# Optimization experiments

Measured on AMD Instinct MI355X. Metric: run time of the kernel, lower is better.

Reference implementation:

```python
import jax, jax.numpy as jnp
import numpy as np

NUM_CLASSES = 2047
TIME_WEIGHT = 2.0
EOS_COEF = 0.1
B, Q, N = 64, 100, 16


def _lsa(cost):
    """Jonker-Volgenant min-cost assignment for rectangular cost [R, C], R <= C.
    Returns (row_ind, col_ind) with row_ind = arange(R). Equivalent to
    scipy.optimize.linear_sum_assignment."""
    R, Cn = cost.shape
    u = np.zeros(R + 1)
    v = np.zeros(Cn + 1)
    p = np.zeros(Cn + 1, dtype=np.int64)  # p[j] = 1-based row matched to col j (0 = free)
    for i in range(1, R + 1):
        p[0] = i
        j0 = 0
        minv = np.full(Cn + 1, np.inf)
        used = np.zeros(Cn + 1, dtype=bool)
        way = np.zeros(Cn + 1, dtype=np.int64)
        while True:
            used[j0] = True
            i0 = p[j0]
            cur = cost[i0 - 1] - u[i0] - v[1:]
            free = ~used[1:]
            upd = free & (cur < minv[1:])
            minv[1:] = np.where(upd, cur, minv[1:])
            way[1:] = np.where(upd, j0, way[1:])
            j1 = int(np.argmin(np.where(free, minv[1:], np.inf))) + 1
            delta = minv[j1]
            u[p[used]] += delta
            v[used] -= delta
            minv[1:] = np.where(free, minv[1:] - delta, minv[1:])
            j0 = j1
            if p[j0] == 0:
                break
        while j0 != 0:  # augment along the alternating path
            j1 = way[j0]
            p[j0] = p[j1]
            j0 = j1
    col4row = np.zeros(R, dtype=np.int64)
    for j in range(1, Cn + 1):
        if p[j] > 0:
            col4row[p[j] - 1] = j - 1
    return np.arange(R), col4row


def _match(C):
    """C: np.ndarray [B, Q, N]. Returns (query_idx [B,N], target_idx [B,N])."""
    b, q, n = C.shape
    qs = np.zeros((b, n), np.int64)
    ts = np.zeros((b, n), np.int64)
    for i in range(b):
        r, c = _lsa(C[i].T)  # rows = targets (N), cols = queries (Q); N <= Q
        ts[i] = r
        qs[i] = c
    return qs, ts


def setup_inputs() -> dict:
    key = jax.random.key(0)
    k1, k2, k3, k4 = jax.random.split(key, 4)
    pred_logits = jax.random.normal(k1, (B, Q, NUM_CLASSES + 1), dtype=jnp.float32)
    pred_time = jax.random.uniform(k2, (B, Q, 1), dtype=jnp.float32)
    labels = jax.random.randint(k3, (B, N), 1, NUM_CLASSES + 1)  # class 0 = no-object
    timestamps = jax.random.uniform(k4, (B, N, 1), dtype=jnp.float32)
    return {"pred_logits": pred_logits, "pred_time": pred_time,
            "labels": labels, "timestamps": timestamps}


def reference(pred_logits, pred_time, labels, timestamps):
    b, q = pred_logits.shape[:2]
    n = labels.shape[1]
    # --- Hungarian matching cost (detached, host-side assignment as in the original) ---
    probs = jax.nn.softmax(pred_logits, axis=-1)                              # [B,Q,C+1]
    cost_class = -jnp.take_along_axis(probs, labels[:, None, :], axis=2)      # [B,Q,N]
    cost_time = jnp.abs(pred_time[..., 0][:, :, None] -
                        timestamps[..., 0][:, None, :])                       # [B,Q,N] (cdist p=1)
    C = cost_class + TIME_WEIGHT * cost_time
    Cnp = np.nan_to_num(np.asarray(jax.device_get(C)),
                        nan=100.0, posinf=100.0, neginf=-100.0)
    qs, ts = _match(Cnp)
    qs_j = jnp.asarray(qs)  # matched query indices  [B,N]
    ts_j = jnp.asarray(ts)  # matched target indices [B,N]
    # --- weighted cross entropy over all queries ---
    class_ids = jnp.take_along_axis(labels, ts_j, axis=1)                     # [B,N]
    batch_ar = jnp.arange(b)[:, None]
    target_classes = jnp.zeros((b, q), dtype=jnp.int64).at[batch_ar, qs_j].set(class_ids)
    logZ = jax.nn.logsumexp(pred_logits, axis=-1)                             # [B,Q]
    tgt_logit = jnp.take_along_axis(pred_logits, target_classes[..., None], axis=2)[..., 0]
    nll = logZ - tgt_logit                                                    # [B,Q]
    ce_w = jnp.ones(NUM_CLASSES + 1, jnp.float32).at[0].set(EOS_COEF)
    w = ce_w[target_classes]
    loss_ce = jnp.sum(w * nll) / jnp.sum(w)
    # --- L1 loss on matched timestamps ---
    matched_pred = pred_time[batch_ar, qs_j, 0]                               # [B,N]
    matched_tgt = jnp.take_along_axis(timestamps[..., 0], ts_j, axis=1)       # [B,N]
    loss_time = jnp.mean(jnp.abs(matched_pred - matched_tgt))
    return loss_ce + TIME_WEIGHT * loss_time
```

## Files before the change

### kernel.cpp

```cpp
#include <hip/hip_runtime.h>
#include <hip/hip_bf16.h>
#include <math.h>

#define BB 64
#define QQ 100
#define NN 16
#define CC 2048
#define TIME_WEIGHT 2.0f
#define EOS_COEF 0.1f

__device__ __forceinline__ double readlane_d(double x, int lane) {
    int lo = __builtin_amdgcn_readlane(__double2loint(x), lane);
    int hi = __builtin_amdgcn_readlane(__double2hiint(x), lane);
    return __hiloint2double(hi, lo);
}

template <int CTRL>
__device__ __forceinline__ double dpp_fmin_f64(double x) {
    int lo_s = __double2loint(x), hi_s = __double2hiint(x);
    int lo = __builtin_amdgcn_update_dpp(lo_s, lo_s, CTRL, 0xF, 0xF, false);
    int hi = __builtin_amdgcn_update_dpp(hi_s, hi_s, CTRL, 0xF, 0xF, false);
    return fmin(x, __hiloint2double(hi, lo));
}

__global__ __launch_bounds__(256) void lse_cost_kernel(
    const float* __restrict__ logits, const float* __restrict__ ptime,
    const int* __restrict__ labels, const float* __restrict__ tstamp,
    float* __restrict__ logZ, float* __restrict__ Cg,
    float* __restrict__ lsepart, float* __restrict__ sums, int* __restrict__ counter)
{
    if (blockIdx.x == 0 && threadIdx.x == 0) {
        sums[0] = 0.f; sums[1] = 0.f; *counter = 0;
    }
    const int wave = threadIdx.x >> 6;
    const int lane = threadIdx.x & 63;
    const int bq = blockIdx.x * 4 + wave;
    const int b = bq / QQ, q = bq % QQ;
    const float4* row4 = (const float4*)(logits + (size_t)bq * CC);

    float4 v[8];
    #pragma unroll
    for (int c = 0; c < 8; ++c) v[c] = row4[c * 64 + lane];

    float m = -INFINITY;
    #pragma unroll
    for (int c = 0; c < 8; ++c)
        m = fmaxf(m, fmaxf(fmaxf(v[c].x, v[c].y), fmaxf(v[c].z, v[c].w)));
    #pragma unroll
    for (int s = 1; s < 64; s <<= 1) m = fmaxf(m, __shfl_xor(m, s, 64));

    float sum = 0.f;
    #pragma unroll
    for (int c = 0; c < 8; ++c)
        sum += expf(v[c].x - m) + expf(v[c].y - m) +
               expf(v[c].z - m) + expf(v[c].w - m);
    #pragma unroll
    for (int s = 1; s < 64; s <<= 1) sum += __shfl_xor(sum, s, 64);

    const float lz = m + logf(sum);
    if (lane == 0) logZ[bq] = lz;

    const float pt = ptime[bq];
    if (lane < NN) {
        int lab = labels[b * NN + lane];
        float lg = logits[(size_t)bq * CC + lab];
        float cc = -expf(lg - lz);
        float ct = fabsf(pt - tstamp[b * NN + lane]);
        float val = cc + TIME_WEIGHT * ct;
        if (isnan(val)) val = 100.0f;
        else if (isinf(val)) val = (val > 0.f) ? 100.0f : -100.0f;
        Cg[((size_t)b * NN + lane) * QQ + q] = val;
    }

    __shared__ float red[4];
    if (lane == 0) red[wave] = lz - logits[(size_t)bq * CC];
    __syncthreads();
    if (threadIdx.x == 0)
        lsepart[blockIdx.x] = red[0] + red[1] + red[2] + red[3];
}

__global__ __launch_bounds__(64) void hungarian_kernel(
    const float* __restrict__ Cg, const float* __restrict__ logits,
    const float* __restrict__ ptime, const int* __restrict__ labels,
    const float* __restrict__ tstamp, const float* __restrict__ logZ,
    const float* __restrict__ lsepart, float* __restrict__ sums,
    int* __restrict__ counter, float* __restrict__ out)
{
    const int b = blockIdx.x;
    const int t = threadIdx.x;

    __shared__ float costS[NN * QQ];
    __shared__ int qsl[NN];

    const float* cgb = Cg + (size_t)b * NN * QQ;
    #pragma unroll
    for (int k = 0; k < 25; ++k) costS[k * 64 + t] = cgb[k * 64 + t];
    __syncthreads();

    const int jc0 = t + 1;
    const int jc1 = t + 65;
    const bool has2 = (jc1 <= QQ);
    const int t2 = has2 ? (t + 64) : t;

    double v0 = 0.0, v1 = 0.0;
    double ureg = 0.0;
    int preg0 = 0, preg1 = 0;
    const double INF = __builtin_inf();

    for (int i = 1; i <= NN; ++i) {
        double minv0 = INF, minv1 = INF;
        bool used0 = false, used1 = false;
        int way0 = 0, way1 = 0;
        bool inTree = (t == i - 1);
        int j0 = 0;
        int i0 = i;

        while (true) {
            used0 |= (j0 == jc0);
            used1 |= (j0 == jc1);
            inTree = inTree || (t == i0 - 1);
            const double u_i0 = readlane_d(ureg, i0 - 1);

            const int rowbase = (i0 - 1) * QQ;
            const double ca = (double)costS[rowbase + t];
            const double cb = (double)costS[rowbase + t2];

            if (!used0) {
                double cur = ca - u_i0 - v0;
                if (cur < minv0) { minv0 = cur; way0 = j0; }
            }
            if (has2 && !used1) {
                double cur = cb - u_i0 - v1;
                if (cur < minv1) { minv1 = cur; way1 = j0; }
            }

            double m0 = used0 ? INF : minv0;
            double m1 = (has2 && !used1) ? minv1 : INF;
            double gmin = fmin(m0, m1);
            gmin = dpp_fmin_f64<0xB1>(gmin);
            gmin = dpp_fmin_f64<0x4E>(gmin);
            gmin = dpp_fmin_f64<0x124>(gmin);
            gmin = dpp_fmin_f64<0x128>(gmin);
            {
                double h0 = readlane_d(gmin, 0);
                double h1 = readlane_d(gmin, 16);
                double h2 = readlane_d(gmin, 32);
                double h3 = readlane_d(gmin, 48);
                gmin = fmin(fmin(h0, h1), fmin(h2, h3));
            }
            unsigned long long A  = __ballot(!used0 && (minv0 == gmin));
            unsigned long long Bm = __ballot(has2 && !used1 && (minv1 == gmin));
            int j1 = (A != 0ull) ? ((int)__builtin_ctzll(A) + 1)
                                 : ((int)__builtin_ctzll(Bm) + 65);
            const double delta = gmin;

            if (inTree) ureg += delta;
            if (used0) v0 -= delta; else minv0 -= delta;
            if (has2) { if (used1) v1 -= delta; else minv1 -= delta; }

            j0 = j1;
            int pj = (j0 <= 64) ? __builtin_amdgcn_readlane(preg0, j0 - 1)
                                : __builtin_amdgcn_readlane(preg1, j0 - 65);
            if (pj == 0) break;
            i0 = pj;
        }

        while (j0 != 0) {
            int jn = (j0 <= 64) ? __builtin_amdgcn_readlane(way0, j0 - 1)
                                : __builtin_amdgcn_readlane(way1, j0 - 65);
            int pv;
            if (jn == 0) pv = i;
            else pv = (jn <= 64) ? __builtin_amdgcn_readlane(preg0, jn - 1)
                                 : __builtin_amdgcn_readlane(preg1, jn - 65);
            if (j0 == jc0) preg0 = pv;
            if (has2 && j0 == jc1) preg1 = pv;
            j0 = jn;
        }
    }

    if (preg0 > 0) qsl[preg0 - 1] = jc0 - 1;
    if (has2 && preg1 > 0) qsl[preg1 - 1] = jc1 - 1;
    __syncthreads();

    float corr = 0.f, tl = 0.f;
    if (t < NN) {
        int qcol = qsl[t];
        int lab = labels[b * NN + t];
        int bq = b * QQ + qcol;
        float lz = logZ[bq];
        float lgm = logits[(size_t)bq * CC + lab];
        float lg0 = logits[(size_t)bq * CC];
        corr = (lz - lgm) - EOS_COEF * (lz - lg0);
        tl = fabsf(ptime[bq] - tstamp[b * NN + t]);
    }
    #pragma unroll
    for (int s = 1; s < 64; s <<= 1) {
        corr += __shfl_xor(corr, s, 64);
        tl   += __shfl_xor(tl, s, 64);
    }

    int old = 0;
    if (t == 0) {
        atomicAdd(&sums[0], corr);
        atomicAdd(&sums[1], tl);
        __threadfence();
        old = atomicAdd(counter, 1);
    }
    old = __shfl(old, 0, 64);
    if (old == BB - 1) {
        __threadfence();
        float r0 = 0.f;
        #pragma unroll
        for (int k = 0; k < 25; ++k) r0 += lsepart[t + 64 * k];
        #pragma unroll
        for (int s = 1; s < 64; s <<= 1) r0 += __shfl_xor(r0, s, 64);
        if (t == 0) {
            float s0 = atomicAdd(&sums[0], 0.0f);
            float s1 = atomicAdd(&sums[1], 0.0f);
            const float sum_w = (float)(BB * NN) * 1.0f
                              + (float)(BB * (QQ - NN)) * EOS_COEF;
            float loss_ce = (EOS_COEF * r0 + s0) / sum_w;
            float loss_t  = s1 / (float)(BB * NN);
            out[0] = loss_ce + TIME_WEIGHT * loss_t;
        }
    }
}

extern "C" void kernel_launch(void* const* d_in, const int* in_sizes, int n_in,
                              void* d_out, int out_size, void* d_ws, size_t ws_size,
                              hipStream_t stream) {
    const float* logits = (const float*)d_in[0];
    const float* ptime  = (const float*)d_in[1];
    const int*   labels = (const int*)d_in[2];
    const float* tstamp = (const float*)d_in[3];
    float* out = (float*)d_out;

    char* ws = (char*)d_ws;
    float* logZ    = (float*)ws;
    float* Cg      = (float*)(ws + 25600);
    float* lsepart = (float*)(ws + 435200);
    float* sums    = (float*)(ws + 441600);
    int*   counter = (int*)(ws + 441608);

    lse_cost_kernel<<<1600, 256, 0, stream>>>(logits, ptime, labels, tstamp,
                                              logZ, Cg, lsepart, sums, counter);
    hungarian_kernel<<<BB, 64, 0, stream>>>(Cg, logits, ptime, labels, tstamp,
                                            logZ, lsepart, sums, counter, out);
}
```

Baseline: 105.4 us.

## Fuse LSE/cost and Hungarian kernels via per-batch last-block election

Merges the two kernels into one launch. The last of the 25 blocks that finish a batch's cost rows, detected with a per-batch atomic counter, runs the Hungarian assignment for that batch. The cost tile is staged as a float2 layout so each lane gets both of its columns in one LDS read. Global atomic sums are replaced by per-batch slots plus a final reduction, and counters are cleared with a memset. This removes a kernel launch and the tail serialization between stages, and lets the assignment of early batches overlap with LSE work on later ones, at the cost of an extra memset node and fence-based cross-block synchronization.

```diff
diff --git a/kernel.cpp b/kernel.cpp
--- a/kernel.cpp
+++ b/kernel.cpp
@@ -23,21 +23,24 @@
     return fmin(x, __hiloint2double(hi, lo));
 }
 
-__global__ __launch_bounds__(256) void lse_cost_kernel(
+__device__ __forceinline__ float load_agent(const float* p) {
+    return __hip_atomic_load((float*)p, __ATOMIC_RELAXED, __HIP_MEMORY_SCOPE_AGENT);
+}
+
+__global__ __launch_bounds__(256) void fused_kernel(
     const float* __restrict__ logits, const float* __restrict__ ptime,
     const int* __restrict__ labels, const float* __restrict__ tstamp,
     float* __restrict__ logZ, float* __restrict__ Cg,
-    float* __restrict__ lsepart, float* __restrict__ sums, int* __restrict__ counter)
+    float* __restrict__ lsepart, float* __restrict__ corrB,
+    float* __restrict__ tlB, int* __restrict__ bcnt,
+    int* __restrict__ counter, float* __restrict__ out)
 {
-    if (blockIdx.x == 0 && threadIdx.x == 0) {
-        sums[0] = 0.f; sums[1] = 0.f; *counter = 0;
-    }
     const int wave = threadIdx.x >> 6;
     const int lane = threadIdx.x & 63;
     const int bq = blockIdx.x * 4 + wave;
     const int b = bq / QQ, q = bq % QQ;
+
     const float4* row4 = (const float4*)(logits + (size_t)bq * CC);
-
     float4 v[8];
     #pragma unroll
     for (int c = 0; c < 8; ++c) v[c] = row4[c * 64 + lane];
@@ -73,34 +76,37 @@
     }
 
     __shared__ float red[4];
+    __shared__ int lastFlag;
     if (lane == 0) red[wave] = lz - logits[(size_t)bq * CC];
+
+    __threadfence();
     __syncthreads();
-    if (threadIdx.x == 0)
+    if (threadIdx.x == 0) {
         lsepart[blockIdx.x] = red[0] + red[1] + red[2] + red[3];
-}
-
-__global__ __launch_bounds__(64) void hungarian_kernel(
-    const float* __restrict__ Cg, const float* __restrict__ logits,
-    const float* __restrict__ ptime, const int* __restrict__ labels,
-    const float* __restrict__ tstamp, const float* __restrict__ logZ,
-    const float* __restrict__ lsepart, float* __restrict__ sums,
-    int* __restrict__ counter, float* __restrict__ out)
-{
-    const int b = blockIdx.x;
+        __threadfence();
+        lastFlag = (atomicAdd(&bcnt[b], 1) == 24);
+    }
+    __syncthreads();
+    if (!lastFlag) return;
+    if (threadIdx.x >= 64) return;
+
     const int t = threadIdx.x;
-
-    __shared__ float costS[NN * QQ];
-    __shared__ int qsl[NN];
-
-    const float* cgb = Cg + (size_t)b * NN * QQ;
-    #pragma unroll
-    for (int k = 0; k < 25; ++k) costS[k * 64 + t] = cgb[k * 64 + t];
-    __syncthreads();
+    __threadfence();
 
     const int jc0 = t + 1;
     const int jc1 = t + 65;
     const bool has2 = (jc1 <= QQ);
     const int t2 = has2 ? (t + 64) : t;
+
+    __shared__ float2 costS2[NN][64];
+    const float* cgb = Cg + (size_t)b * NN * QQ;
+    #pragma unroll
+    for (int r = 0; r < NN; ++r) {
+        float a = load_agent(&cgb[r * QQ + t]);
+        float c = load_agent(&cgb[r * QQ + t2]);
+        costS2[r][t] = make_float2(a, c);
+    }
+    asm volatile("s_waitcnt lgkmcnt(0)" ::: "memory");
 
     double v0 = 0.0, v1 = 0.0;
     double ureg = 0.0;
@@ -121,9 +127,9 @@
             inTree = inTree || (t == i0 - 1);
             const double u_i0 = readlane_d(ureg, i0 - 1);
 
-            const int rowbase = (i0 - 1) * QQ;
-            const double ca = (double)costS[rowbase + t];
-            const double cb = (double)costS[rowbase + t2];
+            const float2 cab = costS2[i0 - 1][t];
+            const double ca = (double)cab.x;
+            const double cb = (double)cab.y;
 
             if (!used0) {
                 double cur = ca - u_i0 - v0;
@@ -178,20 +184,21 @@
         }
     }
 
+    __shared__ int qsl[NN];
     if (preg0 > 0) qsl[preg0 - 1] = jc0 - 1;
     if (has2 && preg1 > 0) qsl[preg1 - 1] = jc1 - 1;
-    __syncthreads();
+    asm volatile("s_waitcnt lgkmcnt(0)" ::: "memory");
 
     float corr = 0.f, tl = 0.f;
     if (t < NN) {
         int qcol = qsl[t];
         int lab = labels[b * NN + t];
-        int bq = b * QQ + qcol;
-        float lz = logZ[bq];
-        float lgm = logits[(size_t)bq * CC + lab];
-        float lg0 = logits[(size_t)bq * CC];
-        corr = (lz - lgm) - EOS_COEF * (lz - lg0);
-        tl = fabsf(ptime[bq] - tstamp[b * NN + t]);
+        int bq2 = b * QQ + qcol;
+        float lz2 = load_agent(&logZ[bq2]);
+        float lgm = logits[(size_t)bq2 * CC + lab];
+        float lg0 = logits[(size_t)bq2 * CC];
+        corr = (lz2 - lgm) - EOS_COEF * (lz2 - lg0);
+        tl = fabsf(ptime[bq2] - tstamp[b * NN + t]);
     }
     #pragma unroll
     for (int s = 1; s < 64; s <<= 1) {
@@ -201,8 +208,8 @@
 
     int old = 0;
     if (t == 0) {
-        atomicAdd(&sums[0], corr);
-        atomicAdd(&sums[1], tl);
+        corrB[b] = corr;
+        tlB[b] = tl;
         __threadfence();
         old = atomicAdd(counter, 1);
     }
@@ -211,12 +218,16 @@
         __threadfence();
         float r0 = 0.f;
         #pragma unroll
-        for (int k = 0; k < 25; ++k) r0 += lsepart[t + 64 * k];
+        for (int k = 0; k < 25; ++k)
+            r0 += load_agent(&lsepart[t + 64 * k]);
         #pragma unroll
         for (int s = 1; s < 64; s <<= 1) r0 += __shfl_xor(r0, s, 64);
         if (t == 0) {
-            float s0 = atomicAdd(&sums[0], 0.0f);
-            float s1 = atomicAdd(&sums[1], 0.0f);
+            float s0 = 0.f, s1 = 0.f;
+            for (int i2 = 0; i2 < BB; ++i2) {
+                s0 += load_agent(&corrB[i2]);
+                s1 += load_agent(&tlB[i2]);
+            }
             const float sum_w = (float)(BB * NN) * 1.0f
                               + (float)(BB * (QQ - NN)) * EOS_COEF;
             float loss_ce = (EOS_COEF * r0 + s0) / sum_w;
@@ -239,11 +250,14 @@
     float* logZ    = (float*)ws;
     float* Cg      = (float*)(ws + 25600);
     float* lsepart = (float*)(ws + 435200);
-    float* sums    = (float*)(ws + 441600);
-    int*   counter = (int*)(ws + 441608);
-
-    lse_cost_kernel<<<1600, 256, 0, stream>>>(logits, ptime, labels, tstamp,
-                                              logZ, Cg, lsepart, sums, counter);
-    hungarian_kernel<<<BB, 64, 0, stream>>>(Cg, logits, ptime, labels, tstamp,
-                                            logZ, lsepart, sums, counter, out);
-}
+    float* corrB   = (float*)(ws + 441600);
+    float* tlB     = (float*)(ws + 441856);
+    int*   bcnt    = (int*)(ws + 442112);
+    int*   counter = (int*)(ws + 442368);
+
+    hipMemsetAsync(ws + 442112, 0, 260, stream);
+
+    fused_kernel<<<1600, 256, 0, stream>>>(logits, ptime, labels, tstamp,
+                                           logZ, Cg, lsepart, corrB, tlB,
+                                           bcnt, counter, out);
+}
```

Result: slower. 271.5 us (+157.6%).

## Pack cost rows as per-lane float2 in LDS, drop barriers, pin logits registers

Applied to the files above, without the earlier changes.

The Hungarian kernel now stores each cost row as a per-lane float2 holding both of that lane's columns, so each augmenting step does one 64-bit LDS read instead of two scalar reads. The __syncthreads barriers are replaced with s_waitcnt lgkmcnt(0). That is enough only because the block is a single wave and each lane reads its own LDS slot. In the LSE kernel, empty asm statements pin the loaded logits in VGPRs so the compiler cannot rematerialize or reorder the loads. The asm and barrier removal depend on wave64 single-wave blocks and rely on compiler and hardware behaviour.

```diff
diff --git a/kernel.cpp b/kernel.cpp
--- a/kernel.cpp
+++ b/kernel.cpp
@@ -1,5 +1,4 @@
 #include <hip/hip_runtime.h>
-#include <hip/hip_bf16.h>
 #include <math.h>
 
 #define BB 64
@@ -22,6 +21,16 @@
     int hi = __builtin_amdgcn_update_dpp(hi_s, hi_s, CTRL, 0xF, 0xF, false);
     return fmin(x, __hiloint2double(hi, lo));
 }
+
+#define KEEP_ALIVE_V8(v)                                                     \
+    asm volatile("" : "+v"(v[0].x), "+v"(v[0].y), "+v"(v[0].z), "+v"(v[0].w),\
+                     "+v"(v[1].x), "+v"(v[1].y), "+v"(v[1].z), "+v"(v[1].w),\
+                     "+v"(v[2].x), "+v"(v[2].y), "+v"(v[2].z), "+v"(v[2].w),\
+                     "+v"(v[3].x), "+v"(v[3].y), "+v"(v[3].z), "+v"(v[3].w));\
+    asm volatile("" : "+v"(v[4].x), "+v"(v[4].y), "+v"(v[4].z), "+v"(v[4].w),\
+                     "+v"(v[5].x), "+v"(v[5].y), "+v"(v[5].z), "+v"(v[5].w),\
+                     "+v"(v[6].x), "+v"(v[6].y), "+v"(v[6].z), "+v"(v[6].w),\
+                     "+v"(v[7].x), "+v"(v[7].y), "+v"(v[7].z), "+v"(v[7].w))
 
 __global__ __launch_bounds__(256) void lse_cost_kernel(
     const float* __restrict__ logits, const float* __restrict__ ptime,
@@ -41,6 +50,7 @@
     float4 v[8];
     #pragma unroll
     for (int c = 0; c < 8; ++c) v[c] = row4[c * 64 + lane];
+    KEEP_ALIVE_V8(v);
 
     float m = -INFINITY;
     #pragma unroll
@@ -48,6 +58,7 @@
         m = fmaxf(m, fmaxf(fmaxf(v[c].x, v[c].y), fmaxf(v[c].z, v[c].w)));
     #pragma unroll
     for (int s = 1; s < 64; s <<= 1) m = fmaxf(m, __shfl_xor(m, s, 64));
+    KEEP_ALIVE_V8(v);
 
     float sum = 0.f;
     #pragma unroll
@@ -89,18 +100,22 @@
     const int b = blockIdx.x;
     const int t = threadIdx.x;
 
-    __shared__ float costS[NN * QQ];
+    __shared__ float2 costS2[NN][64];
     __shared__ int qsl[NN];
-
-    const float* cgb = Cg + (size_t)b * NN * QQ;
-    #pragma unroll
-    for (int k = 0; k < 25; ++k) costS[k * 64 + t] = cgb[k * 64 + t];
-    __syncthreads();
 
     const int jc0 = t + 1;
     const int jc1 = t + 65;
     const bool has2 = (jc1 <= QQ);
     const int t2 = has2 ? (t + 64) : t;
+
+    const float* cgb = Cg + (size_t)b * NN * QQ;
+    #pragma unroll
+    for (int r = 0; r < NN; ++r) {
+        float a = cgb[r * QQ + t];
+        float c = cgb[r * QQ + t2];
+        costS2[r][t] = make_float2(a, c);
+    }
+    asm volatile("s_waitcnt lgkmcnt(0)" ::: "memory");
 
     double v0 = 0.0, v1 = 0.0;
     double ureg = 0.0;
@@ -121,9 +136,9 @@
             inTree = inTree || (t == i0 - 1);
             const double u_i0 = readlane_d(ureg, i0 - 1);
 
-            const int rowbase = (i0 - 1) * QQ;
-            const double ca = (double)costS[rowbase + t];
-            const double cb = (double)costS[rowbase + t2];
+            const float2 cab = costS2[i0 - 1][t];
+            const double ca = (double)cab.x;
+            const double cb = (double)cab.y;
 
             if (!used0) {
                 double cur = ca - u_i0 - v0;
@@ -180,7 +195,7 @@
 
     if (preg0 > 0) qsl[preg0 - 1] = jc0 - 1;
     if (has2 && preg1 > 0) qsl[preg1 - 1] = jc1 - 1;
-    __syncthreads();
+    asm volatile("s_waitcnt lgkmcnt(0)" ::: "memory");
 
     float corr = 0.f, tl = 0.f;
     if (t < NN) {
```

Measured after the change: 103.3 us, median of 2. -2.0%, faster.
